# Kernel optimization log

Hardware: AMD Instinct MI355X
Metric: run time of the kernel (lower is better)

Reference implementation:

```python
import jax, jax.numpy as jnp
import numpy as np

HEADS = 6
POINTS = 4
INJ_SHAPES = ((96, 96), (48, 48), (24, 24))  # adapter pyramid (H_l, W_l), sum = 12096 tokens
EXT_SHAPES = ((48, 48),)                      # vit grid level


def layernorm(x, g, b, eps=1e-6):
    m = jnp.mean(x, axis=-1, keepdims=True)
    v = jnp.mean((x - m) ** 2, axis=-1, keepdims=True)
    return (x - m) * jax.lax.rsqrt(v + eps) * g + b


def bilinear_sample(img, loc):
    # img: [B, heads, H, W, D]; loc: [B, heads, P, 2] normalized (x, y) in [0, 1]
    # matches F.grid_sample(mode='bilinear', padding_mode='zeros', align_corners=False)
    B, nh, H, W, D = img.shape
    flat = img.reshape(B, nh, H * W, D)
    ix = loc[..., 0] * W - 0.5
    iy = loc[..., 1] * H - 0.5
    x0f = jnp.floor(ix)
    y0f = jnp.floor(iy)
    wx = (ix - x0f)[..., None]
    wy = (iy - y0f)[..., None]
    x0 = x0f.astype(jnp.int32)
    y0 = y0f.astype(jnp.int32)

    def gather(xi, yi):
        valid = (xi >= 0) & (xi < W) & (yi >= 0) & (yi < H)
        idx = jnp.clip(yi, 0, H - 1) * W + jnp.clip(xi, 0, W - 1)
        g = jnp.take_along_axis(flat, idx[..., None], axis=2)
        return g * valid[..., None]

    v00 = gather(x0, y0)
    v01 = gather(x0 + 1, y0)
    v10 = gather(x0, y0 + 1)
    v11 = gather(x0 + 1, y0 + 1)
    return (v00 * (1 - wx) + v01 * wx) * (1 - wy) + (v10 * (1 - wx) + v11 * wx) * wy


def msda(query, value, ref, shapes, Wv, bv, Ws, bs_, Wa, ba, Wo, bo):
    # mmcv MultiScaleDeformableAttention (batch_first) without dropout/identity.
    B, Lq, C = query.shape
    D = C // HEADS
    L = len(shapes)
    v = (value @ Wv + bv).reshape(B, -1, HEADS, D)
    off = (query @ Ws + bs_).reshape(B, Lq, HEADS, L, POINTS, 2)
    aw = jax.nn.softmax((query @ Wa + ba).reshape(B, Lq, HEADS, L * POINTS), axis=-1)
    aw = aw.reshape(B, Lq, HEADS, L, POINTS)
    norm = jnp.array([[w, h] for (h, w) in shapes], dtype=query.dtype)  # (x, y) normalizer
    # ref: [B, Lq, 1, 2] broadcasts over heads/levels/points
    loc = ref[:, :, None, :, None, :] + off / norm[None, None, None, :, None, :]
    starts = np.cumsum([0] + [h * w for h, w in shapes])
    out = jnp.zeros((B, HEADS, Lq, D), query.dtype)
    for l, (h, w) in enumerate(shapes):
        vl = v[:, starts[l]:starts[l + 1]].reshape(B, h, w, HEADS, D).transpose(0, 3, 1, 2, 4)
        ll = loc[:, :, :, l].transpose(0, 2, 1, 3, 4).reshape(B, HEADS, Lq * POINTS, 2)
        s = bilinear_sample(vl, ll).reshape(B, HEADS, Lq, POINTS, D)
        out = out + jnp.einsum('bhqp,bhqpd->bhqd', aw[:, :, :, l].transpose(0, 2, 1, 3), s)
    out = out.transpose(0, 2, 1, 3).reshape(B, Lq, C)
    return out @ Wo + bo


def setup_inputs() -> dict:
    key = jax.random.key(0)
    ks = jax.random.split(key, 24)
    B, Hh, Ww, C = 1, 48, 48, 768
    NA = 12096  # 4*HW + HW + HW/4
    f32 = jnp.float32
    lin = lambda k, i, o, s=0.02: jax.random.normal(k, (i, o), f32) * s
    p = {
        'vit_feats': jax.random.normal(ks[0], (B, Hh, Ww, C), f32),
        'adapter_feats': jax.random.normal(ks[1], (B, NA, C), f32),
        'ref1': jax.random.uniform(ks[2], (B, Hh * Ww, 1, 2), f32),
        'ref2': jax.random.uniform(ks[3], (B, NA, 1, 2), f32),
        'inj_qn_g': jnp.ones((C,), f32), 'inj_qn_b': jnp.zeros((C,), f32),
        'inj_Wv': lin(ks[4], C, C), 'inj_bv': jnp.zeros((C,), f32),
        'inj_Ws': lin(ks[5], C, HEADS * 3 * POINTS * 2, 0.01),
        'inj_bs': jax.random.normal(ks[6], (HEADS * 3 * POINTS * 2,), f32),
        'inj_Wa': lin(ks[7], C, HEADS * 3 * POINTS), 'inj_ba': jnp.zeros((HEADS * 3 * POINTS,), f32),
        'inj_Wo': lin(ks[8], C, C), 'inj_bo': jnp.zeros((C,), f32),
        'inj_gamma': jax.random.normal(ks[9], (C,), f32) * 0.1,
        'ext_vn_g': jnp.ones((C,), f32), 'ext_vn_b': jnp.zeros((C,), f32),
        'ext_qn_g': jnp.ones((C,), f32), 'ext_qn_b': jnp.zeros((C,), f32),
        'ext_Wv': lin(ks[10], C, C), 'ext_bv': jnp.zeros((C,), f32),
        'ext_Ws': lin(ks[11], C, HEADS * 1 * POINTS * 2, 0.01),
        'ext_bs': jax.random.normal(ks[12], (HEADS * 1 * POINTS * 2,), f32),
        'ext_Wa': lin(ks[13], C, HEADS * 1 * POINTS), 'ext_ba': jnp.zeros((HEADS * 1 * POINTS,), f32),
        'ext_Wo': lin(ks[14], C, C), 'ext_bo': jnp.zeros((C,), f32),
        'H': 48, 'W': 48,
    }
    return p


def reference(vit_feats, adapter_feats, ref1, ref2,
              inj_qn_g, inj_qn_b, inj_Wv, inj_bv, inj_Ws, inj_bs, inj_Wa, inj_ba, inj_Wo, inj_bo, inj_gamma,
              ext_vn_g, ext_vn_b, ext_qn_g, ext_qn_b, ext_Wv, ext_bv, ext_Ws, ext_bs, ext_Wa, ext_ba, ext_Wo, ext_bo,
              H, W):
    b, h, w, c = vit_feats.shape
    q = vit_feats.reshape(b, h * w, c)
    # Injector: query = vit tokens, value = 3-level adapter pyramid; identity = 0, gamma-scaled residual
    attn = msda(layernorm(q, inj_qn_g, inj_qn_b), adapter_feats, ref1, INJ_SHAPES,
                inj_Wv, inj_bv, inj_Ws, inj_bs, inj_Wa, inj_ba, inj_Wo, inj_bo)
    q = q + inj_gamma * attn
    vit_out = q.reshape(b, h, w, c)
    # Extractor (with_cffn=False, v_pre_norm=True): value = LN(vit tokens), identity = adapter query, post query-norm
    value = layernorm(q, ext_vn_g, ext_vn_b)
    attn2 = msda(adapter_feats, value, ref2, EXT_SHAPES,
                 ext_Wv, ext_bv, ext_Ws, ext_bs, ext_Wa, ext_ba, ext_Wo, ext_bo)
    adapter_out = layernorm(adapter_feats + attn2, ext_qn_g, ext_qn_b)
    return vit_out, adapter_out
```

## Files before the change

kernel.cpp:

```cpp
#include <hip/hip_runtime.h>


#define LQ_VIT 2304
#define NA_ADA 12096

typedef float f32x4 __attribute__((ext_vector_type(4)));
typedef float f32x8 __attribute__((ext_vector_type(8)));
typedef short bf16x8 __attribute__((ext_vector_type(8)));
typedef unsigned short u16x8 __attribute__((ext_vector_type(8)));

__device__ __forceinline__ unsigned short f2bf(float f) {
  unsigned u = __builtin_bit_cast(unsigned, f);
  u += 0x7FFFu + ((u >> 16) & 1u);
  return (unsigned short)(u >> 16);
}
__device__ __forceinline__ float bf2f(unsigned short u) {
  return __builtin_bit_cast(float, (unsigned)u << 16);
}
__device__ __forceinline__ f32x8 ld8bf(const unsigned short* p) {
  u16x8 t = *(const u16x8*)p;
  f32x8 r;
#pragma unroll
  for (int j = 0; j < 8; j++) r[j] = bf2f(t[j]);
  return r;
}

__device__ __forceinline__ void gload_lds16(const void* g, void* l) {
  __builtin_amdgcn_global_load_lds(
      (__attribute__((address_space(1))) void*)(void*)g,
      (__attribute__((address_space(3))) void*)l, 16, 0, 0);
}

#define FENCE() __builtin_amdgcn_sched_barrier(0)
#define WAITV(n) do { asm volatile("s_waitcnt vmcnt(" #n ")" ::: "memory"); } while (0)
#define BAR() do { FENCE(); __builtin_amdgcn_s_barrier(); FENCE(); } while (0)

struct PrepPack {
  const float* W[8];
  unsigned short* WT[8];
  int N[8];
  int cum[9];
  const float* adapter; unsigned short* adbf; int n4;
  const float* vit; const float* qg; const float* qb; unsigned short* qln;
  const float* isv; const float* iav; const float* ibv;
  const float* esv; const float* eav;
  float* bci; float* bbig;
};

__global__ __launch_bounds__(256) void prep_kernel(PrepPack pp) {
  int b = blockIdx.x;
  int tid = threadIdx.x;
  if (b < 2568) {
    int kb = b / 107, col = b % 107;
    int z = 0;
#pragma unroll
    for (int i = 0; i < 8; i++) if (col >= pp.cum[i + 1]) z = i + 1;
    int nb = col - pp.cum[z];
    const float* __restrict__ W = pp.W[z];
    unsigned short* __restrict__ WT = pp.WT[z];
    int N = pp.N[z];
    int kb32 = kb * 32, nb32 = nb * 32;
    __shared__ float tile[32][33];
    int tx = tid & 31, ty = tid >> 5;
    for (int i = ty; i < 32; i += 8) {
      int n = nb32 + tx;
      tile[i][tx] = (n < N) ? W[(size_t)(kb32 + i) * N + n] : 0.f;
    }
    __syncthreads();
    for (int i = ty; i < 32; i += 8) {
      int n = nb32 + i, k = kb32 + tx;
      if (n < N) WT[(size_t)n * 768 + k] = f2bf(tile[tx][i]);
    }
  } else if (b < 4616) {
    for (int i = (b - 2568) * 256 + tid; i < pp.n4; i += 2048 * 256) {
      float4 v = ((const float4*)pp.adapter)[i];
      ushort4 o;
      o.x = f2bf(v.x); o.y = f2bf(v.y); o.z = f2bf(v.z); o.w = f2bf(v.w);
      ((ushort4*)pp.adbf)[i] = o;
    }
  } else if (b < 5192) {
    int wid = (b - 4616) * 4 + (tid >> 6);
    int lane = tid & 63;
    if (wid >= LQ_VIT) return;
    const float* row = pp.vit + (size_t)wid * 768;
    float x[12]; float s = 0.f;
#pragma unroll
    for (int j = 0; j < 12; j++) { x[j] = row[lane + j * 64]; s += x[j]; }
#pragma unroll
    for (int o = 32; o >= 1; o >>= 1) s += __shfl_xor(s, o);
    float mean = s * (1.f / 768.f);
    float v = 0.f;
#pragma unroll
    for (int j = 0; j < 12; j++) { float d = x[j] - mean; v += d * d; }
#pragma unroll
    for (int o = 32; o >= 1; o >>= 1) v += __shfl_xor(v, o);
    float rs = rsqrtf(v * (1.f / 768.f) + 1e-6f);
#pragma unroll
    for (int j = 0; j < 12; j++) {
      int c = lane + j * 64;
      pp.qln[(size_t)wid * 768 + c] = f2bf((x[j] - mean) * rs * pp.qg[c] + pp.qb[c]);
    }
  } else {
    for (int i = tid; i < 840; i += 256) {
      if (i < 144) pp.bci[i] = pp.isv[i];
      else if (i < 216) pp.bci[i] = pp.iav[i - 144];
      if (i < 768) pp.bbig[i] = pp.ibv[i];
      else if (i < 816) pp.bbig[i] = pp.esv[i - 768];
      else pp.bbig[i] = pp.eav[i - 816];
    }
  }
}

struct GemmTask {
  const unsigned short* A; const unsigned short* BT;
  const float* bias; unsigned short* C;
  int M, N, NT, nwg;
};

__global__ __launch_bounds__(512) void gemm_big8_kernel(GemmTask t0, GemmTask t1, int split) {
  __shared__ unsigned short lds[3][(128 + 128) * 32];

  GemmTask tk = (blockIdx.x < split) ? t0 : t1;
  int id = (blockIdx.x < split) ? blockIdx.x : blockIdx.x - split;
  int nwg = tk.nwg;
  int qq = nwg >> 3, rr = nwg & 7;
  int xcd = id & 7, idx = id >> 3;
  int wg = (xcd < rr ? xcd * (qq + 1) : rr * (qq + 1) + (xcd - rr) * qq) + idx;
  int nt = wg % tk.NT, mt = wg / tk.NT;
  int m0 = mt * 128, n0 = nt * 128;
  int M = tk.M, N = tk.N;
  const unsigned short* __restrict__ A = tk.A;
  const unsigned short* __restrict__ BT = tk.BT;
  const int K = 768, kT = 24;

  int tid = threadIdx.x;
  int w = tid >> 6, lane = tid & 63;
  int wr = w >> 2, wc = w & 3;
  int frow = lane & 15, ghi = lane >> 4;
  int sr = lane >> 2;
  int sgx = (((lane & 3) ^ ((lane >> 3) & 3)) * 8);
  int gxr = ((ghi ^ ((frow >> 1) & 3)) * 8);

  f32x4 acc[4][2] = {};

  auto stage = [&](unsigned short* dst, int k0) {
#pragma unroll
    for (int i = 0; i < 2; i++) {
      int c = w * 2 + i;
      if (c < 8) {
        int gm = m0 + c * 16 + sr; if (gm >= M) gm = M - 1;
        gload_lds16(&A[(size_t)gm * K + k0 + sgx], &dst[c * 512]);
      } else {
        int gn = n0 + (c - 8) * 16 + sr; if (gn >= N) gn = N - 1;
        gload_lds16(&BT[(size_t)gn * K + k0 + sgx], &dst[c * 512]);
      }
    }
  };

  stage(&lds[0][0], 0);
  stage(&lds[1][0], 32);
  WAITV(2);
  BAR();

#pragma unroll
  for (int t = 0; t < kT; t++) {
    unsigned short* cb = &lds[t % 3][0];
    if (t + 2 < kT) stage(&lds[(t + 2) % 3][0], (t + 2) << 5);
    const unsigned short* As_ = cb;
    const unsigned short* Bs_ = cb + 128 * 32;
    bf16x8 af[4], bg[2];
#pragma unroll
    for (int m = 0; m < 4; m++)
      af[m] = *(const bf16x8*)&As_[(wr * 64 + m * 16 + frow) * 32 + gxr];
#pragma unroll
    for (int n = 0; n < 2; n++)
      bg[n] = *(const bf16x8*)&Bs_[(wc * 32 + n * 16 + frow) * 32 + gxr];
#pragma unroll
    for (int m = 0; m < 4; m++)
#pragma unroll
      for (int n = 0; n < 2; n++)
        acc[m][n] = __builtin_amdgcn_mfma_f32_16x16x32_bf16(af[m], bg[n], acc[m][n], 0, 0, 0);
    if (t < kT - 1) {
      if (t + 2 < kT) { WAITV(2); }
      else            { WAITV(0); }
      BAR();
    }
  }

  int orow = (lane >> 4) * 4, ocol = lane & 15;
  unsigned short* C = tk.C;
  const float* bias = tk.bias;
#pragma unroll
  for (int m = 0; m < 4; m++) {
    int gmb = m0 + wr * 64 + m * 16 + orow;
#pragma unroll
    for (int n = 0; n < 2; n++) {
      int gn = n0 + wc * 32 + n * 16 + ocol;
      if (gn < N) {
        float bv = bias[gn];
#pragma unroll
        for (int r = 0; r < 4; r++) {
          int gm = gmb + r;
          if (gm < M) C[(size_t)gm * N + gn] = f2bf(acc[m][n][r] + bv);
        }
      }
    }
  }
}

__global__ __launch_bounds__(256) void gemm_mid_kernel(
    const unsigned short* __restrict__ A, const unsigned short* __restrict__ BT,
    const float* __restrict__ bias, unsigned short* __restrict__ C,
    int M, int N, int NT) {
  __shared__ unsigned short lds[3][(64 + 128) * 32];

  int nwg = gridDim.x;
  int id = blockIdx.x;
  int qq = nwg >> 3, rr = nwg & 7;
  int xcd = id & 7, idx = id >> 3;
  int wg = (xcd < rr ? xcd * (qq + 1) : rr * (qq + 1) + (xcd - rr) * qq) + idx;
  int nt = wg % NT, mt = wg / NT;
  int m0 = mt * 64, n0 = nt * 128;
  const int K = 768, kT = 24;

  int tid = threadIdx.x;
  int w = tid >> 6, lane = tid & 63;
  int frow = lane & 15, ghi = lane >> 4;
  int sr = lane >> 2;
  int sgx = (((lane & 3) ^ ((lane >> 3) & 3)) * 8);
  int gxr = ((ghi ^ ((frow >> 1) & 3)) * 8);

  f32x4 acc[4][2] = {};

  auto stage = [&](unsigned short* dst, int k0) {
#pragma unroll
    for (int i = 0; i < 3; i++) {
      int c = w * 3 + i;
      if (c < 4) {
        int gm = m0 + c * 16 + sr; if (gm >= M) gm = M - 1;
        gload_lds16(&A[(size_t)gm * K + k0 + sgx], &dst[c * 512]);
      } else {
        int gn = n0 + (c - 4) * 16 + sr; if (gn >= N) gn = N - 1;
        gload_lds16(&BT[(size_t)gn * K + k0 + sgx], &dst[c * 512]);
      }
    }
  };

  stage(&lds[0][0], 0);
  stage(&lds[1][0], 32);
  WAITV(3);
  BAR();

#pragma unroll
  for (int t = 0; t < kT; t++) {
    unsigned short* cb = &lds[t % 3][0];
    if (t + 2 < kT) stage(&lds[(t + 2) % 3][0], (t + 2) << 5);
    const unsigned short* As_ = cb;
    const unsigned short* Bs_ = cb + 64 * 32;
    bf16x8 af[4], bg[2];
#pragma unroll
    for (int m = 0; m < 4; m++)
      af[m] = *(const bf16x8*)&As_[(m * 16 + frow) * 32 + gxr];
#pragma unroll
    for (int n = 0; n < 2; n++)
      bg[n] = *(const bf16x8*)&Bs_[(w * 32 + n * 16 + frow) * 32 + gxr];
#pragma unroll
    for (int m = 0; m < 4; m++)
#pragma unroll
      for (int n = 0; n < 2; n++)
        acc[m][n] = __builtin_amdgcn_mfma_f32_16x16x32_bf16(af[m], bg[n], acc[m][n], 0, 0, 0);
    if (t < kT - 1) {
      if (t + 2 < kT) { WAITV(3); }
      else            { WAITV(0); }
      BAR();
    }
  }

  int orow = (lane >> 4) * 4, ocol = lane & 15;
#pragma unroll
  for (int m = 0; m < 4; m++) {
    int gmb = m0 + m * 16 + orow;
#pragma unroll
    for (int n = 0; n < 2; n++) {
      int gn = n0 + w * 32 + n * 16 + ocol;
      if (gn < N) {
        float bv = bias[gn];
#pragma unroll
        for (int r = 0; r < 4; r++) {
          int gm = gmb + r;
          if (gm < M) C[(size_t)gm * N + gn] = f2bf(acc[m][n][r] + bv);
        }
      }
    }
  }
}

__global__ __launch_bounds__(256) void residual_ln_kernel(
    const float* __restrict__ vit, const unsigned short* __restrict__ attn,
    const float* __restrict__ gamma, const float* __restrict__ g,
    const float* __restrict__ b, float* __restrict__ vout,
    unsigned short* __restrict__ vln, int R) {
  int wid = blockIdx.x * 4 + (threadIdx.x >> 6);
  int lane = threadIdx.x & 63;
  if (wid >= R) return;
  const float* ra = vit + (size_t)wid * 768;
  const unsigned short* rb = attn + (size_t)wid * 768;
  float x[12]; float s = 0.f;
#pragma unroll
  for (int j = 0; j < 12; j++) {
    int c = lane + j * 64;
    x[j] = ra[c] + gamma[c] * bf2f(rb[c]);
    vout[(size_t)wid * 768 + c] = x[j];
    s += x[j];
  }
#pragma unroll
  for (int o = 32; o >= 1; o >>= 1) s += __shfl_xor(s, o);
  float mean = s * (1.f / 768.f);
  float v = 0.f;
#pragma unroll
  for (int j = 0; j < 12; j++) { float d = x[j] - mean; v += d * d; }
#pragma unroll
  for (int o = 32; o >= 1; o >>= 1) v += __shfl_xor(v, o);
  float rs = rsqrtf(v * (1.f / 768.f) + 1e-6f);
#pragma unroll
  for (int j = 0; j < 12; j++) {
    int c = lane + j * 64;
    vln[(size_t)wid * 768 + c] = f2bf((x[j] - mean) * rs * g[c] + b[c]);
  }
}

__global__ __launch_bounds__(256) void add_ln_f32_kernel(
    const float* __restrict__ Xa, const unsigned short* __restrict__ Xb,
    const float* __restrict__ g, const float* __restrict__ b,
    float* __restrict__ out, int R) {
  int wid = blockIdx.x * 4 + (threadIdx.x >> 6);
  int lane = threadIdx.x & 63;
  if (wid >= R) return;
  const float* ra = Xa + (size_t)wid * 768;
  const unsigned short* rb = Xb + (size_t)wid * 768;
  float x[12]; float s = 0.f;
#pragma unroll
  for (int j = 0; j < 12; j++) {
    int c = lane + j * 64;
    x[j] = ra[c] + bf2f(rb[c]); s += x[j];
  }
#pragma unroll
  for (int o = 32; o >= 1; o >>= 1) s += __shfl_xor(s, o);
  float mean = s * (1.f / 768.f);
  float v = 0.f;
#pragma unroll
  for (int j = 0; j < 12; j++) { float d = x[j] - mean; v += d * d; }
#pragma unroll
  for (int o = 32; o >= 1; o >>= 1) v += __shfl_xor(v, o);
  float rs = rsqrtf(v * (1.f / 768.f) + 1e-6f);
#pragma unroll
  for (int j = 0; j < 12; j++) {
    int c = lane + j * 64;
    out[(size_t)wid * 768 + c] = (x[j] - mean) * rs * g[c] + b[c];
  }
}


__global__ __launch_bounds__(256) void sampler_inj_kernel(
    const float* __restrict__ ref, const unsigned short* __restrict__ sa,
    const unsigned short* __restrict__ v, unsigned short* __restrict__ out, int vst) {
  int gw = (blockIdx.x * 256 + threadIdx.x) >> 6;
  int lane = threadIdx.x & 63;
  int qp = gw / 3, wv = gw - qp * 3;
  int gh = wv * 4 + (lane >> 4);
  int q = qp * 2 + (gh >= 6 ? 1 : 0);
  if (q >= LQ_VIT) return;
  int h = gh >= 6 ? gh - 6 : gh;
  int c = h * 128 + (lane & 15) * 8;
  float rx = ref[q * 2], ry = ref[q * 2 + 1];
  const unsigned short* row = sa + (size_t)q * 216;
  float lg[12]; float mx = -1e30f;
#pragma unroll
  for (int i = 0; i < 12; i++) { lg[i] = bf2f(row[144 + h * 12 + i]); mx = fmaxf(mx, lg[i]); }
  float s = 0.f;
#pragma unroll
  for (int i = 0; i < 12; i++) { lg[i] = __expf(lg[i] - mx); s += lg[i]; }
  float inv = 1.f / s;
  f32x8 acc = {};
  const int LW[3] = {96, 48, 24};
  const int LS[3] = {0, 9216, 11520};
#pragma unroll
  for (int l = 0; l < 3; l++) {
    const int Wl = LW[l], st = LS[l], Wm = Wl - 1;
    const float Wf = (float)Wl;
#pragma unroll
    for (int p = 0; p < 4; p++) {
      int ob = ((h * 3 + l) * 4 + p) * 2;
      float ix = fmaf(rx, Wf, bf2f(row[ob])) - 0.5f;
      float iy = fmaf(ry, Wf, bf2f(row[ob + 1])) - 0.5f;
      float x0f = floorf(ix), y0f = floorf(iy);
      float wx = ix - x0f, wy = iy - y0f;
      int x0 = (int)x0f, y0 = (int)y0f;
      float aw = lg[l * 4 + p] * inv;
      float wy0 = (1.f - wy) * aw, wy1 = wy * aw;
      float w00 = (1.f - wx) * wy0, w01 = wx * wy0;
      float w10 = (1.f - wx) * wy1, w11 = wx * wy1;
      bool xv0 = (unsigned)x0 < (unsigned)Wl, xv1 = (unsigned)(x0 + 1) < (unsigned)Wl;
      bool yv0 = (unsigned)y0 < (unsigned)Wl, yv1 = (unsigned)(y0 + 1) < (unsigned)Wl;
      w00 = (xv0 && yv0) ? w00 : 0.f;
      w01 = (xv1 && yv0) ? w01 : 0.f;
      w10 = (xv0 && yv1) ? w10 : 0.f;
      w11 = (xv1 && yv1) ? w11 : 0.f;
      int x0c = min(max(x0, 0), Wm), x1c = min(max(x0 + 1, 0), Wm);
      int y0c = min(max(y0, 0), Wm), y1c = min(max(y0 + 1, 0), Wm);
      const unsigned short* r0 = v + ((size_t)(st + y0c * Wl) * vst + c);
      const unsigned short* r1 = v + ((size_t)(st + y1c * Wl) * vst + c);
      acc += w00 * ld8bf(r0 + (size_t)x0c * vst) + w01 * ld8bf(r0 + (size_t)x1c * vst)
           + w10 * ld8bf(r1 + (size_t)x0c * vst) + w11 * ld8bf(r1 + (size_t)x1c * vst);
    }
  }
  u16x8 o8;
#pragma unroll
  for (int j = 0; j < 8; j++) o8[j] = f2bf(acc[j]);
  *(u16x8*)&out[(size_t)q * 768 + c] = o8;
}

__global__ __launch_bounds__(256) void sampler_ext_kernel(
    const float* __restrict__ ref, const unsigned short* __restrict__ sa, int sst,
    const unsigned short* __restrict__ v, unsigned short* __restrict__ out) {
  int gw = (blockIdx.x * 256 + threadIdx.x) >> 6;
  int lane = threadIdx.x & 63;
  int qp = gw / 3, wv = gw - qp * 3;
  int gh = wv * 4 + (lane >> 4);
  int q = qp * 2 + (gh >= 6 ? 1 : 0);
  if (q >= NA_ADA) return;
  int h = gh >= 6 ? gh - 6 : gh;
  int c = h * 128 + (lane & 15) * 8;
  float rx = ref[q * 2], ry = ref[q * 2 + 1];
  const unsigned short* row = sa + (size_t)q * sst;
  float lg[4]; float mx = -1e30f;
#pragma unroll
  for (int p = 0; p < 4; p++) { lg[p] = bf2f(row[48 + h * 4 + p]); mx = fmaxf(mx, lg[p]); }
  float s = 0.f;
#pragma unroll
  for (int p = 0; p < 4; p++) { lg[p] = __expf(lg[p] - mx); s += lg[p]; }
  float inv = 1.f / s;
  f32x8 acc = {};
#pragma unroll
  for (int p = 0; p < 4; p++) {
    int ob = (h * 4 + p) * 2;
    float ix = fmaf(rx, 48.f, bf2f(row[ob])) - 0.5f;
    float iy = fmaf(ry, 48.f, bf2f(row[ob + 1])) - 0.5f;
    float x0f = floorf(ix), y0f = floorf(iy);
    float wx = ix - x0f, wy = iy - y0f;
    int x0 = (int)x0f, y0 = (int)y0f;
    float aw = lg[p] * inv;
    float wy0 = (1.f - wy) * aw, wy1 = wy * aw;
    float w00 = (1.f - wx) * wy0, w01 = wx * wy0;
    float w10 = (1.f - wx) * wy1, w11 = wx * wy1;
    bool xv0 = (unsigned)x0 < 48u, xv1 = (unsigned)(x0 + 1) < 48u;
    bool yv0 = (unsigned)y0 < 48u, yv1 = (unsigned)(y0 + 1) < 48u;
    w00 = (xv0 && yv0) ? w00 : 0.f;
    w01 = (xv1 && yv0) ? w01 : 0.f;
    w10 = (xv0 && yv1) ? w10 : 0.f;
    w11 = (xv1 && yv1) ? w11 : 0.f;
    int x0c = min(max(x0, 0), 47), x1c = min(max(x0 + 1, 0), 47);
    int y0c = min(max(y0, 0), 47), y1c = min(max(y0 + 1, 0), 47);
    const unsigned short* r0 = v + ((size_t)(y0c * 48) * 768 + c);
    const unsigned short* r1 = v + ((size_t)(y1c * 48) * 768 + c);
    acc += w00 * ld8bf(r0 + (size_t)x0c * 768) + w01 * ld8bf(r0 + (size_t)x1c * 768)
         + w10 * ld8bf(r1 + (size_t)x0c * 768) + w11 * ld8bf(r1 + (size_t)x1c * 768);
  }
  u16x8 o8;
#pragma unroll
  for (int j = 0; j < 8; j++) o8[j] = f2bf(acc[j]);
  *(u16x8*)&out[(size_t)q * 768 + c] = o8;
}

extern "C" void kernel_launch(void* const* d_in, const int* in_sizes, int n_in,
                              void* d_out, int out_size, void* d_ws, size_t ws_size,
                              hipStream_t stream) {
  (void)in_sizes; (void)n_in; (void)out_size; (void)ws_size;
  const float* vit      = (const float*)d_in[0];
  const float* adapter  = (const float*)d_in[1];
  const float* ref1     = (const float*)d_in[2];
  const float* ref2     = (const float*)d_in[3];
  const float* inj_qn_g = (const float*)d_in[4];
  const float* inj_qn_b = (const float*)d_in[5];
  const float* inj_Wv   = (const float*)d_in[6];
  const float* inj_bv   = (const float*)d_in[7];
  const float* inj_Ws   = (const float*)d_in[8];
  const float* inj_bs   = (const float*)d_in[9];
  const float* inj_Wa   = (const float*)d_in[10];
  const float* inj_ba   = (const float*)d_in[11];
  const float* inj_Wo   = (const float*)d_in[12];
  const float* inj_bo   = (const float*)d_in[13];
  const float* inj_gamma= (const float*)d_in[14];
  const float* ext_vn_g = (const float*)d_in[15];
  const float* ext_vn_b = (const float*)d_in[16];
  const float* ext_qn_g = (const float*)d_in[17];
  const float* ext_qn_b = (const float*)d_in[18];
  const float* ext_Wv   = (const float*)d_in[19];
  const float* ext_bv   = (const float*)d_in[20];
  const float* ext_Ws   = (const float*)d_in[21];
  const float* ext_bs   = (const float*)d_in[22];
  const float* ext_Wa   = (const float*)d_in[23];
  const float* ext_ba   = (const float*)d_in[24];
  const float* ext_Wo   = (const float*)d_in[25];
  const float* ext_bo   = (const float*)d_in[26];

  size_t cur = 0;
  auto take = [&](size_t bytes) {
    void* p = (char*)d_ws + cur;
    cur += (bytes + 255) & ~(size_t)255;
    return p;
  };
  unsigned short* WBIG = (unsigned short*)take((size_t)840 * 768 * 2);
  unsigned short* WTIO = (unsigned short*)take((size_t)768 * 768 * 2);
  unsigned short* WTEV = (unsigned short*)take((size_t)768 * 768 * 2);
  unsigned short* WTEO = (unsigned short*)take((size_t)768 * 768 * 2);
  unsigned short* WSAI = (unsigned short*)take((size_t)216 * 768 * 2);
  float* BCI  = (float*)take((size_t)216 * 4);
  float* BBIG = (float*)take((size_t)840 * 4);
  unsigned short* ADBF = (unsigned short*)take((size_t)NA_ADA * 768 * 2);
  unsigned short* QLN  = (unsigned short*)take((size_t)LQ_VIT * 768 * 2);
  unsigned short* CBIG = (unsigned short*)take((size_t)NA_ADA * 840 * 2);
  unsigned short* SAI  = (unsigned short*)take((size_t)LQ_VIT * 216 * 2);
  unsigned short* SAMPI= (unsigned short*)take((size_t)LQ_VIT * 768 * 2);
  unsigned short* ATTNI= (unsigned short*)take((size_t)LQ_VIT * 768 * 2);
  unsigned short* VLN  = (unsigned short*)take((size_t)LQ_VIT * 768 * 2);
  unsigned short* VEXT = (unsigned short*)take((size_t)LQ_VIT * 768 * 2);
  unsigned short* SAMPE = ADBF;
  unsigned short* ATTN2 = CBIG;

  float* out_vit = (float*)d_out;
  float* out_ada = out_vit + (size_t)LQ_VIT * 768;

  PrepPack pp;
  pp.W[0] = inj_Wv; pp.WT[0] = WBIG;               pp.N[0] = 768;
  pp.W[1] = ext_Ws; pp.WT[1] = WBIG + 768 * 768;   pp.N[1] = 48;
  pp.W[2] = ext_Wa; pp.WT[2] = WBIG + 816 * 768;   pp.N[2] = 24;
  pp.W[3] = inj_Wo; pp.WT[3] = WTIO;               pp.N[3] = 768;
  pp.W[4] = ext_Wv; pp.WT[4] = WTEV;               pp.N[4] = 768;
  pp.W[5] = ext_Wo; pp.WT[5] = WTEO;               pp.N[5] = 768;
  pp.W[6] = inj_Ws; pp.WT[6] = WSAI;               pp.N[6] = 144;
  pp.W[7] = inj_Wa; pp.WT[7] = WSAI + 144 * 768;   pp.N[7] = 72;
  int cum = 0;
  for (int i = 0; i < 8; i++) { pp.cum[i] = cum; cum += (pp.N[i] + 31) / 32; }
  pp.cum[8] = cum;
  pp.adapter = adapter; pp.adbf = ADBF; pp.n4 = (NA_ADA * 768) / 4;
  pp.vit = vit; pp.qg = inj_qn_g; pp.qb = inj_qn_b; pp.qln = QLN;
  pp.isv = inj_bs; pp.iav = inj_ba; pp.ibv = inj_bv;
  pp.esv = ext_bs; pp.eav = ext_ba;
  pp.bci = BCI; pp.bbig = BBIG;
  prep_kernel<<<5193, 256, 0, stream>>>(pp);

  GemmTask tA, tB;
  tA.A = ADBF; tA.BT = WBIG; tA.bias = BBIG; tA.C = CBIG;
  tA.M = NA_ADA; tA.N = 840; tA.NT = 7; tA.nwg = 95 * 7;
  tB.A = QLN; tB.BT = WSAI; tB.bias = BCI; tB.C = SAI;
  tB.M = LQ_VIT; tB.N = 216; tB.NT = 2; tB.nwg = 18 * 2;
  gemm_big8_kernel<<<95 * 7 + 18 * 2, 512, 0, stream>>>(tA, tB, 95 * 7);

  sampler_inj_kernel<<<864, 256, 0, stream>>>(ref1, SAI, CBIG, SAMPI, 840);

  gemm_mid_kernel<<<36 * 6, 256, 0, stream>>>(SAMPI, WTIO, inj_bo, ATTNI, LQ_VIT, 768, 6);
  residual_ln_kernel<<<576, 256, 0, stream>>>(vit, ATTNI, inj_gamma, ext_vn_g, ext_vn_b,
                                              out_vit, VLN, LQ_VIT);
  gemm_mid_kernel<<<36 * 6, 256, 0, stream>>>(VLN, WTEV, ext_bv, VEXT, LQ_VIT, 768, 6);

  sampler_ext_kernel<<<4536, 256, 0, stream>>>(ref2, CBIG + 768, 840, VEXT, SAMPE);

  GemmTask tC;
  tC.A = SAMPE; tC.BT = WTEO; tC.bias = ext_bo; tC.C = ATTN2;
  tC.M = NA_ADA; tC.N = 768; tC.NT = 6; tC.nwg = 95 * 6;
  gemm_big8_kernel<<<95 * 6, 512, 0, stream>>>(tC, tC, 95 * 6);

  add_ln_f32_kernel<<<3024, 256, 0, stream>>>(adapter, ATTN2, ext_qn_g, ext_qn_b, out_ada, NA_ADA);
}
```

Baseline: 160.5 us.

## Use 8-wave mid GEMM, add MFMA setprio, vectorize layernorm kernels

Converts the 64x128 mid GEMM from 4 waves to 8 waves, with each wave computing a 32x32 sub-tile and staging split unevenly across waves. This is meant to raise latency hiding on a small 216-block grid. It also wraps the MFMA block in s_setprio for the first big GEMM launch only, and turns the residual/layernorm kernels' scalar loads and stores into float4/ushort4 accesses. The per-wave wait counts now differ by wave index, which adds complexity and some risk of ordering mistakes.

```diff
diff --git a/kernel.cpp b/kernel.cpp
--- a/kernel.cpp
+++ b/kernel.cpp
@@ -117,7 +117,8 @@
   int M, N, NT, nwg;
 };
 
-__global__ __launch_bounds__(512) void gemm_big8_kernel(GemmTask t0, GemmTask t1, int split) {
+__global__ __launch_bounds__(512) void gemm_big8_kernel(GemmTask t0, GemmTask t1,
+                                                        int split, int prio) {
   __shared__ unsigned short lds[3][(128 + 128) * 32];
 
   GemmTask tk = (blockIdx.x < split) ? t0 : t1;
@@ -175,11 +176,13 @@
 #pragma unroll
     for (int n = 0; n < 2; n++)
       bg[n] = *(const bf16x8*)&Bs_[(wc * 32 + n * 16 + frow) * 32 + gxr];
+    if (prio) __builtin_amdgcn_s_setprio(1);
 #pragma unroll
     for (int m = 0; m < 4; m++)
 #pragma unroll
       for (int n = 0; n < 2; n++)
         acc[m][n] = __builtin_amdgcn_mfma_f32_16x16x32_bf16(af[m], bg[n], acc[m][n], 0, 0, 0);
+    if (prio) __builtin_amdgcn_s_setprio(0);
     if (t < kT - 1) {
       if (t + 2 < kT) { WAITV(2); }
       else            { WAITV(0); }
@@ -208,7 +211,7 @@
   }
 }
 
-__global__ __launch_bounds__(256) void gemm_mid_kernel(
+__global__ __launch_bounds__(512) void gemm_mid8_kernel(
     const unsigned short* __restrict__ A, const unsigned short* __restrict__ BT,
     const float* __restrict__ bias, unsigned short* __restrict__ C,
     int M, int N, int NT) {
@@ -225,17 +228,18 @@
 
   int tid = threadIdx.x;
   int w = tid >> 6, lane = tid & 63;
+  int wr = w >> 2, wc = w & 3;
   int frow = lane & 15, ghi = lane >> 4;
   int sr = lane >> 2;
   int sgx = (((lane & 3) ^ ((lane >> 3) & 3)) * 8);
   int gxr = ((ghi ^ ((frow >> 1) & 3)) * 8);
-
-  f32x4 acc[4][2] = {};
+  int wu = __builtin_amdgcn_readfirstlane(w);
+
+  f32x4 acc[2][2] = {};
 
   auto stage = [&](unsigned short* dst, int k0) {
-#pragma unroll
-    for (int i = 0; i < 3; i++) {
-      int c = w * 3 + i;
+    {
+      int c = w;
       if (c < 4) {
         int gm = m0 + c * 16 + sr; if (gm >= M) gm = M - 1;
         gload_lds16(&A[(size_t)gm * K + k0 + sgx], &dst[c * 512]);
@@ -244,11 +248,16 @@
         gload_lds16(&BT[(size_t)gn * K + k0 + sgx], &dst[c * 512]);
       }
     }
+    if (w < 4) {
+      int c = 8 + w;
+      int gn = n0 + (c - 4) * 16 + sr; if (gn >= N) gn = N - 1;
+      gload_lds16(&BT[(size_t)gn * K + k0 + sgx], &dst[c * 512]);
+    }
   };
 
   stage(&lds[0][0], 0);
   stage(&lds[1][0], 32);
-  WAITV(3);
+  if (wu < 4) { WAITV(2); } else { WAITV(1); }
   BAR();
 
 #pragma unroll
@@ -257,20 +266,20 @@
     if (t + 2 < kT) stage(&lds[(t + 2) % 3][0], (t + 2) << 5);
     const unsigned short* As_ = cb;
     const unsigned short* Bs_ = cb + 64 * 32;
-    bf16x8 af[4], bg[2];
-#pragma unroll
-    for (int m = 0; m < 4; m++)
-      af[m] = *(const bf16x8*)&As_[(m * 16 + frow) * 32 + gxr];
+    bf16x8 af[2], bg[2];
+#pragma unroll
+    for (int m = 0; m < 2; m++)
+      af[m] = *(const bf16x8*)&As_[(wr * 32 + m * 16 + frow) * 32 + gxr];
 #pragma unroll
     for (int n = 0; n < 2; n++)
-      bg[n] = *(const bf16x8*)&Bs_[(w * 32 + n * 16 + frow) * 32 + gxr];
-#pragma unroll
-    for (int m = 0; m < 4; m++)
+      bg[n] = *(const bf16x8*)&Bs_[(wc * 32 + n * 16 + frow) * 32 + gxr];
+#pragma unroll
+    for (int m = 0; m < 2; m++)
 #pragma unroll
       for (int n = 0; n < 2; n++)
         acc[m][n] = __builtin_amdgcn_mfma_f32_16x16x32_bf16(af[m], bg[n], acc[m][n], 0, 0, 0);
     if (t < kT - 1) {
-      if (t + 2 < kT) { WAITV(3); }
+      if (t + 2 < kT) { if (wu < 4) { WAITV(2); } else { WAITV(1); } }
       else            { WAITV(0); }
       BAR();
     }
@@ -278,11 +287,11 @@
 
   int orow = (lane >> 4) * 4, ocol = lane & 15;
 #pragma unroll
-  for (int m = 0; m < 4; m++) {
-    int gmb = m0 + m * 16 + orow;
+  for (int m = 0; m < 2; m++) {
+    int gmb = m0 + wr * 32 + m * 16 + orow;
 #pragma unroll
     for (int n = 0; n < 2; n++) {
-      int gn = n0 + w * 32 + n * 16 + ocol;
+      int gn = n0 + wc * 32 + n * 16 + ocol;
       if (gn < N) {
         float bv = bias[gn];
 #pragma unroll
@@ -303,15 +312,24 @@
   int wid = blockIdx.x * 4 + (threadIdx.x >> 6);
   int lane = threadIdx.x & 63;
   if (wid >= R) return;
-  const float* ra = vit + (size_t)wid * 768;
-  const unsigned short* rb = attn + (size_t)wid * 768;
+  const float4* ra = (const float4*)(vit + (size_t)wid * 768);
+  const ushort4* rb = (const ushort4*)(attn + (size_t)wid * 768);
+  float4* vo = (float4*)(vout + (size_t)wid * 768);
+  ushort4* vl = (ushort4*)(vln + (size_t)wid * 768);
   float x[12]; float s = 0.f;
 #pragma unroll
-  for (int j = 0; j < 12; j++) {
-    int c = lane + j * 64;
-    x[j] = ra[c] + gamma[c] * bf2f(rb[c]);
-    vout[(size_t)wid * 768 + c] = x[j];
-    s += x[j];
+  for (int j = 0; j < 3; j++) {
+    int c4 = lane + j * 64;
+    float4 a = ra[c4];
+    ushort4 t = rb[c4];
+    float4 gm = ((const float4*)gamma)[c4];
+    x[j*4+0] = a.x + gm.x * bf2f(t.x);
+    x[j*4+1] = a.y + gm.y * bf2f(t.y);
+    x[j*4+2] = a.z + gm.z * bf2f(t.z);
+    x[j*4+3] = a.w + gm.w * bf2f(t.w);
+    float4 o; o.x = x[j*4+0]; o.y = x[j*4+1]; o.z = x[j*4+2]; o.w = x[j*4+3];
+    vo[c4] = o;
+    s += x[j*4+0] + x[j*4+1] + x[j*4+2] + x[j*4+3];
   }
 #pragma unroll
   for (int o = 32; o >= 1; o >>= 1) s += __shfl_xor(s, o);
@@ -323,9 +341,16 @@
   for (int o = 32; o >= 1; o >>= 1) v += __shfl_xor(v, o);
   float rs = rsqrtf(v * (1.f / 768.f) + 1e-6f);
 #pragma unroll
-  for (int j = 0; j < 12; j++) {
-    int c = lane + j * 64;
-    vln[(size_t)wid * 768 + c] = f2bf((x[j] - mean) * rs * g[c] + b[c]);
+  for (int j = 0; j < 3; j++) {
+    int c4 = lane + j * 64;
+    float4 gg = ((const float4*)g)[c4];
+    float4 bb = ((const float4*)b)[c4];
+    ushort4 o;
+    o.x = f2bf((x[j*4+0] - mean) * rs * gg.x + bb.x);
+    o.y = f2bf((x[j*4+1] - mean) * rs * gg.y + bb.y);
+    o.z = f2bf((x[j*4+2] - mean) * rs * gg.z + bb.z);
+    o.w = f2bf((x[j*4+3] - mean) * rs * gg.w + bb.w);
+    vl[c4] = o;
   }
 }
 
@@ -336,13 +361,20 @@
   int wid = blockIdx.x * 4 + (threadIdx.x >> 6);
   int lane = threadIdx.x & 63;
   if (wid >= R) return;
-  const float* ra = Xa + (size_t)wid * 768;
-  const unsigned short* rb = Xb + (size_t)wid * 768;
+  const float4* ra = (const float4*)(Xa + (size_t)wid * 768);
+  const ushort4* rb = (const ushort4*)(Xb + (size_t)wid * 768);
+  float4* ro = (float4*)(out + (size_t)wid * 768);
   float x[12]; float s = 0.f;
 #pragma unroll
-  for (int j = 0; j < 12; j++) {
-    int c = lane + j * 64;
-    x[j] = ra[c] + bf2f(rb[c]); s += x[j];
+  for (int j = 0; j < 3; j++) {
+    int c4 = lane + j * 64;
+    float4 a = ra[c4];
+    ushort4 t = rb[c4];
+    x[j*4+0] = a.x + bf2f(t.x);
+    x[j*4+1] = a.y + bf2f(t.y);
+    x[j*4+2] = a.z + bf2f(t.z);
+    x[j*4+3] = a.w + bf2f(t.w);
+    s += x[j*4+0] + x[j*4+1] + x[j*4+2] + x[j*4+3];
   }
 #pragma unroll
   for (int o = 32; o >= 1; o >>= 1) s += __shfl_xor(s, o);
@@ -354,12 +386,18 @@
   for (int o = 32; o >= 1; o >>= 1) v += __shfl_xor(v, o);
   float rs = rsqrtf(v * (1.f / 768.f) + 1e-6f);
 #pragma unroll
-  for (int j = 0; j < 12; j++) {
-    int c = lane + j * 64;
-    out[(size_t)wid * 768 + c] = (x[j] - mean) * rs * g[c] + b[c];
-  }
-}
-
+  for (int j = 0; j < 3; j++) {
+    int c4 = lane + j * 64;
+    float4 gg = ((const float4*)g)[c4];
+    float4 bb = ((const float4*)b)[c4];
+    float4 o;
+    o.x = (x[j*4+0] - mean) * rs * gg.x + bb.x;
+    o.y = (x[j*4+1] - mean) * rs * gg.y + bb.y;
+    o.z = (x[j*4+2] - mean) * rs * gg.z + bb.z;
+    o.w = (x[j*4+3] - mean) * rs * gg.w + bb.w;
+    ro[c4] = o;
+  }
+}
 
 __global__ __launch_bounds__(256) void sampler_inj_kernel(
     const float* __restrict__ ref, const unsigned short* __restrict__ sa,
@@ -555,21 +593,21 @@
   tA.M = NA_ADA; tA.N = 840; tA.NT = 7; tA.nwg = 95 * 7;
   tB.A = QLN; tB.BT = WSAI; tB.bias = BCI; tB.C = SAI;
   tB.M = LQ_VIT; tB.N = 216; tB.NT = 2; tB.nwg = 18 * 2;
-  gemm_big8_kernel<<<95 * 7 + 18 * 2, 512, 0, stream>>>(tA, tB, 95 * 7);
+  gemm_big8_kernel<<<95 * 7 + 18 * 2, 512, 0, stream>>>(tA, tB, 95 * 7, 1);
 
   sampler_inj_kernel<<<864, 256, 0, stream>>>(ref1, SAI, CBIG, SAMPI, 840);
 
-  gemm_mid_kernel<<<36 * 6, 256, 0, stream>>>(SAMPI, WTIO, inj_bo, ATTNI, LQ_VIT, 768, 6);
+  gemm_mid8_kernel<<<36 * 6, 512, 0, stream>>>(SAMPI, WTIO, inj_bo, ATTNI, LQ_VIT, 768, 6);
   residual_ln_kernel<<<576, 256, 0, stream>>>(vit, ATTNI, inj_gamma, ext_vn_g, ext_vn_b,
                                               out_vit, VLN, LQ_VIT);
-  gemm_mid_kernel<<<36 * 6, 256, 0, stream>>>(VLN, WTEV, ext_bv, VEXT, LQ_VIT, 768, 6);
+  gemm_mid8_kernel<<<36 * 6, 512, 0, stream>>>(VLN, WTEV, ext_bv, VEXT, LQ_VIT, 768, 6);
 
   sampler_ext_kernel<<<4536, 256, 0, stream>>>(ref2, CBIG + 768, 840, VEXT, SAMPE);
 
   GemmTask tC;
   tC.A = SAMPE; tC.BT = WTEO; tC.bias = ext_bo; tC.C = ATTN2;
   tC.M = NA_ADA; tC.N = 768; tC.NT = 6; tC.nwg = 95 * 6;
-  gemm_big8_kernel<<<95 * 6, 512, 0, stream>>>(tC, tC, 95 * 6);
+  gemm_big8_kernel<<<95 * 6, 512, 0, stream>>>(tC, tC, 95 * 6, 0);
 
   add_ln_f32_kernel<<<3024, 256, 0, stream>>>(adapter, ATTN2, ext_qn_g, ext_qn_b, out_ada, NA_ADA);
 }
```

Measured after the change: 154.9 us. 1.04x faster.
